# Optimization experiments

Hardware: AMD Instinct MI355X
Metric: run time of the kernel (lower is better)

The kernel has to match this reference:

```python
import jax, jax.numpy as jnp
import numpy as np

N_IN = 16384
G = 64            # input grid resolution
K_UP = 8          # 2^3 children per voxel for kernel=2 stride=2 generative transpose conv
N_OUT = N_IN * K_UP
G2 = 2 * G        # output grid resolution
NUMS = 32768      # top-k prune budget
C = 64


def _np_coords_and_maps():
    """Build voxel coords, the 27-offset kernel map on upsampled coords, and a fake GT mask."""
    rng = np.random.default_rng(0)
    flat = rng.choice(G ** 3, size=N_IN, replace=False)
    c = np.stack(np.unravel_index(flat, (G, G, G)), axis=1).astype(np.int64)  # [N_IN,3]
    offs2 = np.stack(np.meshgrid(*([[0, 1]] * 3), indexing='ij'), -1).reshape(-1, 3)  # [8,3]
    cu = (2 * c[:, None, :] + offs2[None]).reshape(-1, 3)  # [N_OUT,3], order n*8+k
    lut = np.full(G2 ** 3, N_OUT, dtype=np.int64)
    key = (cu[:, 0] * G2 + cu[:, 1]) * G2 + cu[:, 2]
    lut[key] = np.arange(N_OUT)
    offs3 = np.stack(np.meshgrid(*([[-1, 0, 1]] * 3), indexing='ij'), -1).reshape(-1, 3)  # [27,3]
    nbr = np.empty((27, N_OUT), np.int64)
    for k, d in enumerate(offs3):
        q = cu + d
        valid = ((q >= 0) & (q < G2)).all(1)
        qk = np.where(valid, (q[:, 0] * G2 + q[:, 1]) * G2 + q[:, 2], 0)
        nbr[k] = np.where(valid, lut[qk], N_OUT)  # N_OUT = sentinel 'missing'
    gt = rng.random(N_OUT) < 0.3  # isin(out.C, ground_truth.C) membership mask
    return nbr.astype(np.int32), gt


def setup_inputs() -> dict:
    key = jax.random.key(0)
    ks = jax.random.split(key, 10)
    nbr, gt = _np_coords_and_maps()
    s = 0.05
    rn = lambda k, shape: jax.random.normal(k, shape, jnp.float32) * s
    z = lambda shape: jnp.zeros(shape, jnp.float32)
    return {
        "x_feats": jax.random.normal(ks[0], (N_IN, C), jnp.float32),
        "Wup": rn(ks[1], (K_UP, C, C)), "bup": z((C,)),
        "Wc0": rn(ks[2], (27, C, C)), "bc0": z((C,)),
        "W00": rn(ks[3], (3, 27, C, C // 4)), "b00": z((3, C // 4)),
        "W01": rn(ks[4], (3, 27, C // 4, C // 2)), "b01": z((3, C // 2)),
        "W10": rn(ks[5], (3, C, C // 4)), "b10": z((3, C // 4)),
        "W11": rn(ks[6], (3, 27, C // 4, C // 4)), "b11": z((3, C // 4)),
        "W12": rn(ks[7], (3, C // 4, C // 2)), "b12": z((3, C // 2)),
        "Wcls": rn(ks[8], (27, C, 1)), "bcls": z((1,)),
        "nbr_idx": jnp.asarray(nbr), "mask_true": jnp.asarray(gt),
        "nums": NUMS,
    }


def sparse_conv(feats, nbr, W, b):
    """Gather-GEMM-scatter sparse conv: feats [N,Cin], nbr [K,N] (N = missing), W [K,Cin,Cout]."""
    fp = jnp.concatenate([feats, jnp.zeros((1, feats.shape[1]), feats.dtype)], axis=0)
    def body(acc, wn):
        Wk, nk = wn
        return acc + fp[nk] @ Wk, None
    acc0 = jnp.zeros((feats.shape[0], W.shape[-1]), feats.dtype)
    out, _ = jax.lax.scan(body, acc0, (W, nbr))
    return out + b


def reference(x_feats, Wup, bup, Wc0, bc0, W00, b00, W01, b01, W10, b10, W11, b11, W12, b12, Wcls, bcls, nbr_idx, mask_true, nums):
    # generative transpose conv k=2 s=2: each voxel emits 8 children (no overlaps)
    up = jnp.einsum('nc,kcd->nkd', x_feats, Wup).reshape(-1, Wup.shape[-1]) + bup  # [N_OUT,C]
    out = jax.nn.relu(up)
    out = jax.nn.relu(sparse_conv(out, nbr_idx, Wc0, bc0))
    for i in range(3):  # 3 InceptionResNet blocks
        o0 = sparse_conv(jax.nn.relu(sparse_conv(out, nbr_idx, W00[i], b00[i])), nbr_idx, W01[i], b01[i])
        t = jax.nn.relu(out @ W10[i] + b10[i])            # 1x1 conv
        t = jax.nn.relu(sparse_conv(t, nbr_idx, W11[i], b11[i]))
        o1 = t @ W12[i] + b12[i]                          # 1x1 conv
        out = jnp.concatenate([o0, o1], axis=1) + out
    out_cls = sparse_conv(out, nbr_idx, Wcls, bcls)       # [N_OUT,1]
    _, idx = jax.lax.top_k(out_cls[:, 0], nums)           # istopk
    mask = jnp.zeros((out.shape[0],), bool).at[idx].set(True) | mask_true  # topk + isin(GT)
    pruned = out * mask[:, None].astype(out.dtype)        # pruning as mask (static shape)
    return out_cls, pruned, mask
```

## Files before the change

kernel.cpp:

```cpp
#include <hip/hip_runtime.h>
#include <cstdint>

#define NOUTC 131072
#define NINC  16384

using uint = unsigned int;

__device__ __forceinline__ uint fkey(float v){
  uint u = __float_as_uint(v);
  return (u & 0x80000000u) ? ~u : (u | 0x80000000u);
}

template<int ROWS, int CIN, int COUT, int TR, int TC, int NK, bool IDENT, bool RELU, bool RESID>
__global__ __launch_bounds__(256)
void spconv(const float* __restrict__ feats,
            const int*   __restrict__ nbr,
            const float* __restrict__ Wg,
            const float* __restrict__ bias,
            const float* __restrict__ resid,
            float*       __restrict__ outp,
            int ostride, int coff)
{
  static_assert(TR == 4, "TR must be 4");
  static_assert((ROWS / TR) * (COUT / TC) == 256, "thread tiling must cover 256 threads");
  constexpr int TPR = 256 / ROWS;
  static_assert(ROWS * TPR == 256, "");
  constexpr int GV = CIN / (4 * TPR);
  static_assert(CIN % (4 * TPR) == 0, "");
  constexpr int STR = ROWS + 4;

  __shared__ float Wl[CIN * COUT];
  __shared__ float ft[CIN][STR];

  const int t    = threadIdx.x;
  const int base = blockIdx.x * ROWS;

  constexpr int CT = COUT / TC;
  const int tcc = (t % CT) * TC;
  const int trr = (t / CT) * TR;

  const int gr    = t / TPR;
  const int gpart = t % TPR;

  float acc[TR][TC];
  #pragma unroll
  for (int a = 0; a < TR; ++a)
    #pragma unroll
    for (int b = 0; b < TC; ++b) acc[a][b] = 0.f;

  for (int k = 0; k < NK; ++k) {
    #pragma unroll
    for (int i = t; i < CIN * COUT; i += 256) Wl[i] = Wg[k * CIN * COUT + i];
    int gidx = IDENT ? (base + gr) : nbr[(size_t)k * NOUTC + base + gr];
    const float4* src = reinterpret_cast<const float4*>(feats + (size_t)gidx * CIN) + gpart * GV;
    #pragma unroll
    for (int j = 0; j < GV; ++j) {
      float4 v = src[j];
      int ci = (gpart * GV + j) * 4;
      ft[ci + 0][gr] = v.x; ft[ci + 1][gr] = v.y;
      ft[ci + 2][gr] = v.z; ft[ci + 3][gr] = v.w;
    }
    __syncthreads();
    #pragma unroll
    for (int ci = 0; ci < CIN; ++ci) {
      float4 f = *reinterpret_cast<const float4*>(&ft[ci][trr]);
      float fv[4] = {f.x, f.y, f.z, f.w};
      float wv[TC];
      if constexpr (TC == 4) {
        float4 w = *reinterpret_cast<const float4*>(&Wl[ci * COUT + tcc]);
        wv[0] = w.x; wv[1] = w.y; wv[2] = w.z; wv[3] = w.w;
      } else {
        float2 w = *reinterpret_cast<const float2*>(&Wl[ci * COUT + tcc]);
        wv[0] = w.x; wv[1] = w.y;
      }
      #pragma unroll
      for (int a = 0; a < TR; ++a)
        #pragma unroll
        for (int b = 0; b < TC; ++b)
          acc[a][b] = fmaf(fv[a], wv[b], acc[a][b]);
    }
    __syncthreads();
  }

  #pragma unroll
  for (int a = 0; a < TR; ++a) {
    int rr = base + trr + a;
    float o[TC];
    #pragma unroll
    for (int b = 0; b < TC; ++b) {
      float v = acc[a][b] + bias[tcc + b];
      if (RELU) v = v > 0.f ? v : 0.f;
      o[b] = v;
    }
    if (RESID) {
      #pragma unroll
      for (int b = 0; b < TC; ++b)
        o[b] += resid[(size_t)rr * 64 + coff + tcc + b];
    }
    float* dst = outp + (size_t)rr * ostride + coff + tcc;
    if constexpr (TC == 4) {
      float4 w4 = {o[0], o[1], o[2], o[3]};
      *reinterpret_cast<float4*>(dst) = w4;
    } else {
      float2 w2 = {o[0], o[1]};
      *reinterpret_cast<float2*>(dst) = w2;
    }
  }
}

__global__ __launch_bounds__(256)
void upsample_kernel(const float* __restrict__ x, const float* __restrict__ Wup,
                     const float* __restrict__ bup, float* __restrict__ outp)
{
  __shared__ float Wl[64 * 64];
  __shared__ float xt[64][68];
  const int t    = threadIdx.x;
  const int tile = blockIdx.x >> 3;
  const int k    = blockIdx.x & 7;
  const int base = tile * 64;

  #pragma unroll
  for (int i = t; i < 4096; i += 256) Wl[i] = Wup[k * 4096 + i];
  {
    const int gr = t >> 2, gp = t & 3;
    const float4* src = reinterpret_cast<const float4*>(x + (size_t)(base + gr) * 64) + gp * 4;
    #pragma unroll
    for (int j = 0; j < 4; ++j) {
      float4 v = src[j];
      int ci = (gp * 4 + j) * 4;
      xt[ci + 0][gr] = v.x; xt[ci + 1][gr] = v.y;
      xt[ci + 2][gr] = v.z; xt[ci + 3][gr] = v.w;
    }
  }
  __syncthreads();
  const int tcc = (t % 16) * 4, trr = (t / 16) * 4;
  float acc[4][4];
  #pragma unroll
  for (int a = 0; a < 4; ++a)
    #pragma unroll
    for (int b = 0; b < 4; ++b) acc[a][b] = 0.f;
  #pragma unroll
  for (int ci = 0; ci < 64; ++ci) {
    float4 f = *reinterpret_cast<const float4*>(&xt[ci][trr]);
    float4 w = *reinterpret_cast<const float4*>(&Wl[ci * 64 + tcc]);
    float fv[4] = {f.x, f.y, f.z, f.w};
    float wv[4] = {w.x, w.y, w.z, w.w};
    #pragma unroll
    for (int a = 0; a < 4; ++a)
      #pragma unroll
      for (int b = 0; b < 4; ++b) acc[a][b] = fmaf(fv[a], wv[b], acc[a][b]);
  }
  #pragma unroll
  for (int a = 0; a < 4; ++a) {
    int n = base + trr + a;
    float4 o;
    float v0 = acc[a][0] + bup[tcc + 0]; o.x = v0 > 0.f ? v0 : 0.f;
    float v1 = acc[a][1] + bup[tcc + 1]; o.y = v1 > 0.f ? v1 : 0.f;
    float v2 = acc[a][2] + bup[tcc + 2]; o.z = v2 > 0.f ? v2 : 0.f;
    float v3 = acc[a][3] + bup[tcc + 3]; o.w = v3 > 0.f ? v3 : 0.f;
    *reinterpret_cast<float4*>(outp + ((size_t)n * 8 + k) * 64 + tcc) = o;
  }
}

__global__ __launch_bounds__(256)
void cls_kernel(const float* __restrict__ feats, const int* __restrict__ nbr,
                const float* __restrict__ Wcls, const float* __restrict__ bcls,
                float* __restrict__ out_cls)
{
  const int wave = threadIdx.x >> 6;
  const int lane = threadIdx.x & 63;
  float wreg[27];
  #pragma unroll
  for (int k = 0; k < 27; ++k) wreg[k] = Wcls[k * 64 + lane];
  const int base = blockIdx.x * 32 + wave * 8;
  for (int rr = 0; rr < 8; ++rr) {
    const int n = base + rr;
    float s = 0.f;
    #pragma unroll
    for (int k = 0; k < 27; ++k) {
      int idx = nbr[(size_t)k * NOUTC + n];
      s = fmaf(feats[(size_t)idx * 64 + lane], wreg[k], s);
    }
    #pragma unroll
    for (int off = 32; off >= 1; off >>= 1) s += __shfl_xor(s, off, 64);
    if (lane == 0) out_cls[n] = s + bcls[0];
  }
}

__global__ void init_kernel(uint* hist1, uint* hist2, int* tie_cnt, int* flag,
                            float* fa, float* fb, float* t0, float* t1)
{
  int i = blockIdx.x * 256 + threadIdx.x;
  if (i < 65536) hist1[i] = 0;
  else if (i < 131072) hist2[i - 65536] = 0;
  if (i == 0) { tie_cnt[0] = 0; flag[0] = 0; }
  if (i < 64) { fa[(size_t)NOUTC * 64 + i] = 0.f; fb[(size_t)NOUTC * 64 + i] = 0.f; }
  if (i < 16) { t0[(size_t)NOUTC * 16 + i] = 0.f; t1[(size_t)NOUTC * 16 + i] = 0.f; }
}

__global__ void detect_kernel(const unsigned char* __restrict__ mt, int* flag)
{
  int i = blockIdx.x * 256 + threadIdx.x;
  int p = i * 4 + 1;
  if (p < NOUTC && mt[p] != 0) flag[0] = 1;
}

__global__ void hist1_kernel(const float* __restrict__ cls, uint* __restrict__ hist)
{
  for (int i = blockIdx.x * blockDim.x + threadIdx.x; i < NOUTC; i += gridDim.x * blockDim.x)
    atomicAdd(&hist[fkey(cls[i]) >> 16], 1u);
}

__global__ void scan1_kernel(const uint* __restrict__ hist, const int* __restrict__ nums,
                             uint* __restrict__ res)
{
  __shared__ uint chunk[256];
  const int t = threadIdx.x;
  uint s = 0;
  for (int j = 0; j < 256; ++j) s += hist[t * 256 + j];
  chunk[t] = s;
  __syncthreads();
  if (t == 0) {
    uint k = (uint)nums[0];
    uint cum = 0; int c = 255;
    for (; c > 0; --c) { if (cum + chunk[c] >= k) break; cum += chunk[c]; }
    int B = c * 256; uint cum2 = cum;
    for (int b = c * 256 + 255; b >= c * 256; --b) {
      if (cum2 + hist[b] >= k) { B = b; break; }
      cum2 += hist[b];
    }
    res[0] = (uint)B; res[1] = cum2;
  }
}

__global__ void hist2_kernel(const float* __restrict__ cls, const uint* __restrict__ res1,
                             uint* __restrict__ hist)
{
  const uint B = res1[0];
  for (int i = blockIdx.x * blockDim.x + threadIdx.x; i < NOUTC; i += gridDim.x * blockDim.x) {
    uint key = fkey(cls[i]);
    if ((key >> 16) == B) atomicAdd(&hist[key & 0xffffu], 1u);
  }
}

__global__ void scan2_kernel(const uint* __restrict__ hist, const uint* __restrict__ res1,
                             const int* __restrict__ nums, uint* __restrict__ res2)
{
  __shared__ uint chunk[256];
  const int t = threadIdx.x;
  uint s = 0;
  for (int j = 0; j < 256; ++j) s += hist[t * 256 + j];
  chunk[t] = s;
  __syncthreads();
  if (t == 0) {
    uint k = (uint)nums[0];
    uint cum = res1[1]; int c = 255;
    for (; c > 0; --c) { if (cum + chunk[c] >= k) break; cum += chunk[c]; }
    int L = c * 256; uint cum2 = cum;
    for (int b = c * 256 + 255; b >= c * 256; --b) {
      if (cum2 + hist[b] >= k) { L = b; break; }
      cum2 += hist[b];
    }
    res2[0] = (res1[0] << 16) | (uint)L;
    res2[1] = k - cum2;
  }
}

__global__ void mark_kernel(const float* __restrict__ cls, const uint* __restrict__ res2,
                            unsigned char* __restrict__ msel, int* tie_cnt, int* tie_idx)
{
  const uint T = res2[0];
  for (int i = blockIdx.x * blockDim.x + threadIdx.x; i < NOUTC; i += gridDim.x * blockDim.x) {
    uint key = fkey(cls[i]);
    msel[i] = key > T ? 1 : 0;
    if (key == T) {
      int p = atomicAdd(tie_cnt, 1);
      if (p < 4096) tie_idx[p] = i;
    }
  }
}

__global__ void tie_kernel(const uint* __restrict__ res2, const int* __restrict__ tie_cnt,
                           const int* __restrict__ tie_idx, unsigned char* __restrict__ msel)
{
  int need = (int)res2[1];
  int cnt = tie_cnt[0]; if (cnt > 4096) cnt = 4096;
  if (need <= 0) return;
  if (cnt <= need) {
    for (int i = threadIdx.x; i < cnt; i += 256) msel[tie_idx[i]] = 1;
  } else {
    for (int i = threadIdx.x; i < cnt; i += 256) {
      int my = tie_idx[i];
      int rank = 0;
      for (int j = 0; j < cnt; ++j) rank += (tie_idx[j] < my) ? 1 : 0;
      if (rank < need) msel[my] = 1;
    }
  }
}

__global__ void prune_kernel(const float* __restrict__ feats, const unsigned char* __restrict__ msel,
                             const void* __restrict__ mtrue, const int* __restrict__ flag,
                             float* __restrict__ dout)
{
  const unsigned char* mb = (const unsigned char*)mtrue;
  const int* mi = (const int*)mtrue;
  const bool bytes = (flag[0] != 0);
  float* pruned = dout + NOUTC;
  float* maskf  = dout + NOUTC + (size_t)NOUTC * 64;
  const float4* src = reinterpret_cast<const float4*>(feats);
  float4* dst = reinterpret_cast<float4*>(pruned);
  const int total = NOUTC * 16;
  for (int i = blockIdx.x * blockDim.x + threadIdx.x; i < total; i += gridDim.x * blockDim.x) {
    int n = i >> 4;
    bool mt = bytes ? (mb[n] != 0) : (mi[n] != 0);
    bool m = (msel[n] != 0) || mt;
    float4 v = src[i];
    float4 z = {0.f, 0.f, 0.f, 0.f};
    dst[i] = m ? v : z;
    if ((i & 15) == 0) maskf[n] = m ? 1.f : 0.f;
  }
}

extern "C" void kernel_launch(void* const* d_in, const int* in_sizes, int n_in,
                              void* d_out, int out_size, void* d_ws, size_t ws_size,
                              hipStream_t stream)
{
  const float* x    = (const float*)d_in[0];
  const float* Wup  = (const float*)d_in[1];
  const float* bup  = (const float*)d_in[2];
  const float* Wc0  = (const float*)d_in[3];
  const float* bc0  = (const float*)d_in[4];
  const float* W00  = (const float*)d_in[5];
  const float* b00  = (const float*)d_in[6];
  const float* W01  = (const float*)d_in[7];
  const float* b01  = (const float*)d_in[8];
  const float* W10  = (const float*)d_in[9];
  const float* b10  = (const float*)d_in[10];
  const float* W11  = (const float*)d_in[11];
  const float* b11  = (const float*)d_in[12];
  const float* W12  = (const float*)d_in[13];
  const float* b12  = (const float*)d_in[14];
  const float* Wcls = (const float*)d_in[15];
  const float* bcls = (const float*)d_in[16];
  const int*   nbr  = (const int*)d_in[17];
  const void*  mtrue= d_in[18];
  const int*   nums = (const int*)d_in[19];

  float* dout = (float*)d_out;

  float* fa = (float*)d_ws;
  float* t0 = fa + (size_t)(NOUTC + 1) * 64;
  float* t1 = t0 + (size_t)(NOUTC + 1) * 16;
  uint*  hist1 = (uint*)(t1 + (size_t)(NOUTC + 1) * 16);
  uint*  hist2 = hist1 + 65536;
  uint*  res1  = hist2 + 65536;
  uint*  res2  = res1 + 2;
  int*   tie_cnt = (int*)(res2 + 2);
  int*   flag    = tie_cnt + 1;
  int*   tie_idx = flag + 1;
  unsigned char* msel = (unsigned char*)(tie_idx + 4096);
  float* fb = dout + NOUTC;

  init_kernel<<<512, 256, 0, stream>>>(hist1, hist2, tie_cnt, flag, fa, fb, t0, t1);
  detect_kernel<<<128, 256, 0, stream>>>((const unsigned char*)mtrue, flag);

  upsample_kernel<<<2048, 256, 0, stream>>>(x, Wup, bup, fa);
  spconv<64, 64, 64, 4, 4, 27, false, true, false>
      <<<NOUTC / 64, 256, 0, stream>>>(fa, nbr, Wc0, bc0, nullptr, fb, 64, 0);

  const float* cur = fb; float* nxt = fa;
  for (int i = 0; i < 3; ++i) {
    spconv<128, 64, 16, 4, 2, 27, false, true, false>
        <<<NOUTC / 128, 256, 0, stream>>>(cur, nbr, W00 + (size_t)i * 27 * 64 * 16,
                                          b00 + i * 16, nullptr, t0, 16, 0);
    spconv<128, 16, 32, 4, 4, 27, false, false, true>
        <<<NOUTC / 128, 256, 0, stream>>>(t0, nbr, W01 + (size_t)i * 27 * 16 * 32,
                                          b01 + i * 32, cur, nxt, 64, 0);
    spconv<128, 64, 16, 4, 2, 1, true, true, false>
        <<<NOUTC / 128, 256, 0, stream>>>(cur, nullptr, W10 + (size_t)i * 64 * 16,
                                          b10 + i * 16, nullptr, t1, 16, 0);
    spconv<128, 16, 16, 4, 2, 27, false, true, false>
        <<<NOUTC / 128, 256, 0, stream>>>(t1, nbr, W11 + (size_t)i * 27 * 16 * 16,
                                          b11 + i * 16, nullptr, t0, 16, 0);
    spconv<128, 16, 32, 4, 4, 1, true, false, true>
        <<<NOUTC / 128, 256, 0, stream>>>(t0, nullptr, W12 + (size_t)i * 16 * 32,
                                          b12 + i * 32, cur, nxt, 64, 32);
    float* tmp = (float*)cur; cur = nxt; nxt = tmp;
  }

  cls_kernel<<<NOUTC / 32, 256, 0, stream>>>(cur, nbr, Wcls, bcls, dout);

  hist1_kernel<<<512, 256, 0, stream>>>(dout, hist1);
  scan1_kernel<<<1, 256, 0, stream>>>(hist1, nums, res1);
  hist2_kernel<<<512, 256, 0, stream>>>(dout, res1, hist2);
  scan2_kernel<<<1, 256, 0, stream>>>(hist2, res1, nums, res2);
  mark_kernel<<<512, 256, 0, stream>>>(dout, res2, msel, tie_cnt, tie_idx);
  tie_kernel<<<1, 256, 0, stream>>>(res2, tie_cnt, tie_idx, msel);
  prune_kernel<<<4096, 256, 0, stream>>>(cur, msel, mtrue, flag, dout);
}
```

Measured before the change: 1.547 ms.

## Replace tiled spconv with one-row-per-thread fused kernels and split cls gather

Swaps the LDS-tiled sparse conv template for kernels where each thread owns one output row, keeps all output channels in registers and reads weights from global/uniform memory. Within each block it fuses the 3x3 and 1x1 branches: W00 and W10 share one gather pass, and W01, W11 and W12 plus the residual share another, which cuts launches and intermediate traffic. The classifier becomes a per-row dot product against all 27 weight slices followed by a scalar gather-sum. Block indices are swizzled. The cost is very high register pressure (64-float accumulators), lower occupancy, and weight loads no longer shared through LDS.

```diff
diff --git a/kernel.cpp b/kernel.cpp
--- a/kernel.cpp
+++ b/kernel.cpp
@@ -11,180 +11,274 @@
   return (u & 0x80000000u) ? ~u : (u | 0x80000000u);
 }
 
-template<int ROWS, int CIN, int COUT, int TR, int TC, int NK, bool IDENT, bool RELU, bool RESID>
-__global__ __launch_bounds__(256)
-void spconv(const float* __restrict__ feats,
-            const int*   __restrict__ nbr,
-            const float* __restrict__ Wg,
-            const float* __restrict__ bias,
-            const float* __restrict__ resid,
-            float*       __restrict__ outp,
-            int ostride, int coff)
-{
-  static_assert(TR == 4, "TR must be 4");
-  static_assert((ROWS / TR) * (COUT / TC) == 256, "thread tiling must cover 256 threads");
-  constexpr int TPR = 256 / ROWS;
-  static_assert(ROWS * TPR == 256, "");
-  constexpr int GV = CIN / (4 * TPR);
-  static_assert(CIN % (4 * TPR) == 0, "");
-  constexpr int STR = ROWS + 4;
-
-  __shared__ float Wl[CIN * COUT];
-  __shared__ float ft[CIN][STR];
-
-  const int t    = threadIdx.x;
-  const int base = blockIdx.x * ROWS;
-
-  constexpr int CT = COUT / TC;
-  const int tcc = (t % CT) * TC;
-  const int trr = (t / CT) * TR;
-
-  const int gr    = t / TPR;
-  const int gpart = t % TPR;
-
-  float acc[TR][TC];
-  #pragma unroll
-  for (int a = 0; a < TR; ++a)
+__device__ __forceinline__ int swz_row(int bx, int tid) {
+  return ((((bx & 7) << 6) | (bx >> 3)) << 8) + tid;
+}
+
+__global__ __launch_bounds__(256)
+void conv_c0_kernel(const float* __restrict__ feats, const int* __restrict__ nbr,
+                    const float* __restrict__ Wg, const float* __restrict__ bias,
+                    float* __restrict__ outp)
+{
+  const int n = swz_row(blockIdx.x, threadIdx.x);
+  float acc[64];
+  #pragma unroll
+  for (int i = 0; i < 64; ++i) acc[i] = 0.f;
+
+  for (int k = 0; k < 27; ++k) {
+    const int idx = nbr[(size_t)k * NOUTC + n];
+    const float4* src = reinterpret_cast<const float4*>(feats + (size_t)idx * 64);
+    const float* w = Wg + k * 4096;
+    #pragma unroll 1
+    for (int c = 0; c < 4; ++c) {
+      float4 a0 = src[c * 4 + 0], a1 = src[c * 4 + 1];
+      float4 a2 = src[c * 4 + 2], a3 = src[c * 4 + 3];
+      float fr[16];
+      fr[0]=a0.x; fr[1]=a0.y; fr[2]=a0.z; fr[3]=a0.w;
+      fr[4]=a1.x; fr[5]=a1.y; fr[6]=a1.z; fr[7]=a1.w;
+      fr[8]=a2.x; fr[9]=a2.y; fr[10]=a2.z; fr[11]=a2.w;
+      fr[12]=a3.x; fr[13]=a3.y; fr[14]=a3.z; fr[15]=a3.w;
+      const float* wc = w + c * 1024;
+      #pragma unroll
+      for (int u = 0; u < 16; ++u)
+        #pragma unroll
+        for (int co = 0; co < 64; ++co)
+          acc[co] = fmaf(fr[u], wc[u * 64 + co], acc[co]);
+    }
+  }
+
+  float* dst = outp + (size_t)n * 64;
+  #pragma unroll
+  for (int j = 0; j < 16; ++j) {
+    float4 o;
+    float v0 = acc[4*j+0] + bias[4*j+0]; o.x = v0 > 0.f ? v0 : 0.f;
+    float v1 = acc[4*j+1] + bias[4*j+1]; o.y = v1 > 0.f ? v1 : 0.f;
+    float v2 = acc[4*j+2] + bias[4*j+2]; o.z = v2 > 0.f ? v2 : 0.f;
+    float v3 = acc[4*j+3] + bias[4*j+3]; o.w = v3 > 0.f ? v3 : 0.f;
+    reinterpret_cast<float4*>(dst)[j] = o;
+  }
+}
+
+__global__ __launch_bounds__(256)
+void conv_A_kernel(const float* __restrict__ feats, const int* __restrict__ nbr,
+                   const float* __restrict__ W00i, const float* __restrict__ b00i,
+                   const float* __restrict__ W10i, const float* __restrict__ b10i,
+                   float* __restrict__ t0, float* __restrict__ t1)
+{
+  const int n = swz_row(blockIdx.x, threadIdx.x);
+  float acc0[16], acc1[16];
+  #pragma unroll
+  for (int i = 0; i < 16; ++i) { acc0[i] = 0.f; acc1[i] = 0.f; }
+
+  for (int k = 0; k < 27; ++k) {
+    const int idx = nbr[(size_t)k * NOUTC + n];
+    const float4* src = reinterpret_cast<const float4*>(feats + (size_t)idx * 64);
+    const float* w0 = W00i + k * 1024;
+    #pragma unroll 1
+    for (int c = 0; c < 4; ++c) {
+      float4 a0 = src[c * 4 + 0], a1 = src[c * 4 + 1];
+      float4 a2 = src[c * 4 + 2], a3 = src[c * 4 + 3];
+      float fr[16];
+      fr[0]=a0.x; fr[1]=a0.y; fr[2]=a0.z; fr[3]=a0.w;
+      fr[4]=a1.x; fr[5]=a1.y; fr[6]=a1.z; fr[7]=a1.w;
+      fr[8]=a2.x; fr[9]=a2.y; fr[10]=a2.z; fr[11]=a2.w;
+      fr[12]=a3.x; fr[13]=a3.y; fr[14]=a3.z; fr[15]=a3.w;
+      #pragma unroll
+      for (int u = 0; u < 16; ++u)
+        #pragma unroll
+        for (int co = 0; co < 16; ++co)
+          acc0[co] = fmaf(fr[u], w0[(c * 16 + u) * 16 + co], acc0[co]);
+      if (k == 13) {
+        #pragma unroll
+        for (int u = 0; u < 16; ++u)
+          #pragma unroll
+          for (int co = 0; co < 16; ++co)
+            acc1[co] = fmaf(fr[u], W10i[(c * 16 + u) * 16 + co], acc1[co]);
+      }
+    }
+  }
+
+  float* d0 = t0 + (size_t)n * 16;
+  float* d1 = t1 + (size_t)n * 16;
+  #pragma unroll
+  for (int j = 0; j < 4; ++j) {
+    float4 o0, o1;
+    float v;
+    v = acc0[4*j+0] + b00i[4*j+0]; o0.x = v > 0.f ? v : 0.f;
+    v = acc0[4*j+1] + b00i[4*j+1]; o0.y = v > 0.f ? v : 0.f;
+    v = acc0[4*j+2] + b00i[4*j+2]; o0.z = v > 0.f ? v : 0.f;
+    v = acc0[4*j+3] + b00i[4*j+3]; o0.w = v > 0.f ? v : 0.f;
+    v = acc1[4*j+0] + b10i[4*j+0]; o1.x = v > 0.f ? v : 0.f;
+    v = acc1[4*j+1] + b10i[4*j+1]; o1.y = v > 0.f ? v : 0.f;
+    v = acc1[4*j+2] + b10i[4*j+2]; o1.z = v > 0.f ? v : 0.f;
+    v = acc1[4*j+3] + b10i[4*j+3]; o1.w = v > 0.f ? v : 0.f;
+    reinterpret_cast<float4*>(d0)[j] = o0;
+    reinterpret_cast<float4*>(d1)[j] = o1;
+  }
+}
+
+__global__ __launch_bounds__(256)
+void conv_B_kernel(const float* __restrict__ t0, const float* __restrict__ t1,
+                   const float* __restrict__ cur, const int* __restrict__ nbr,
+                   const float* __restrict__ W01i, const float* __restrict__ b01i,
+                   const float* __restrict__ W11i, const float* __restrict__ b11i,
+                   const float* __restrict__ W12i, const float* __restrict__ b12i,
+                   float* __restrict__ nxt)
+{
+  const int n = swz_row(blockIdx.x, threadIdx.x);
+  float acc01[32], acc11[16];
+  #pragma unroll
+  for (int i = 0; i < 32; ++i) acc01[i] = 0.f;
+  #pragma unroll
+  for (int i = 0; i < 16; ++i) acc11[i] = 0.f;
+
+  for (int k = 0; k < 27; ++k) {
+    const int idx = nbr[(size_t)k * NOUTC + n];
+    const float4* s0 = reinterpret_cast<const float4*>(t0 + (size_t)idx * 16);
+    const float4* s1 = reinterpret_cast<const float4*>(t1 + (size_t)idx * 16);
+    float4 a0 = s0[0], a1 = s0[1], a2 = s0[2], a3 = s0[3];
+    float4 c0 = s1[0], c1 = s1[1], c2 = s1[2], c3 = s1[3];
+    float f0[16], f1[16];
+    f0[0]=a0.x; f0[1]=a0.y; f0[2]=a0.z; f0[3]=a0.w;
+    f0[4]=a1.x; f0[5]=a1.y; f0[6]=a1.z; f0[7]=a1.w;
+    f0[8]=a2.x; f0[9]=a2.y; f0[10]=a2.z; f0[11]=a2.w;
+    f0[12]=a3.x; f0[13]=a3.y; f0[14]=a3.z; f0[15]=a3.w;
+    f1[0]=c0.x; f1[1]=c0.y; f1[2]=c0.z; f1[3]=c0.w;
+    f1[4]=c1.x; f1[5]=c1.y; f1[6]=c1.z; f1[7]=c1.w;
+    f1[8]=c2.x; f1[9]=c2.y; f1[10]=c2.z; f1[11]=c2.w;
+    f1[12]=c3.x; f1[13]=c3.y; f1[14]=c3.z; f1[15]=c3.w;
+    const float* w01 = W01i + k * 512;
+    const float* w11 = W11i + k * 256;
     #pragma unroll
-    for (int b = 0; b < TC; ++b) acc[a][b] = 0.f;
-
-  for (int k = 0; k < NK; ++k) {
+    for (int u = 0; u < 16; ++u)
+      #pragma unroll
+      for (int co = 0; co < 32; ++co)
+        acc01[co] = fmaf(f0[u], w01[u * 32 + co], acc01[co]);
     #pragma unroll
-    for (int i = t; i < CIN * COUT; i += 256) Wl[i] = Wg[k * CIN * COUT + i];
-    int gidx = IDENT ? (base + gr) : nbr[(size_t)k * NOUTC + base + gr];
-    const float4* src = reinterpret_cast<const float4*>(feats + (size_t)gidx * CIN) + gpart * GV;
+    for (int u = 0; u < 16; ++u)
+      #pragma unroll
+      for (int co = 0; co < 16; ++co)
+        acc11[co] = fmaf(f1[u], w11[u * 16 + co], acc11[co]);
+  }
+
+  float t2[16];
+  #pragma unroll
+  for (int u = 0; u < 16; ++u) {
+    float v = acc11[u] + b11i[u];
+    t2[u] = v > 0.f ? v : 0.f;
+  }
+  float acc12[32];
+  #pragma unroll
+  for (int co = 0; co < 32; ++co) acc12[co] = b12i[co];
+  #pragma unroll
+  for (int u = 0; u < 16; ++u)
     #pragma unroll
-    for (int j = 0; j < GV; ++j) {
-      float4 v = src[j];
-      int ci = (gpart * GV + j) * 4;
-      ft[ci + 0][gr] = v.x; ft[ci + 1][gr] = v.y;
-      ft[ci + 2][gr] = v.z; ft[ci + 3][gr] = v.w;
-    }
-    __syncthreads();
+    for (int co = 0; co < 32; ++co)
+      acc12[co] = fmaf(t2[u], W12i[u * 32 + co], acc12[co]);
+
+  const float4* rs = reinterpret_cast<const float4*>(cur + (size_t)n * 64);
+  float* dst = nxt + (size_t)n * 64;
+  #pragma unroll
+  for (int j = 0; j < 8; ++j) {
+    float4 r = rs[j];
+    float4 o;
+    o.x = acc01[4*j+0] + b01i[4*j+0] + r.x;
+    o.y = acc01[4*j+1] + b01i[4*j+1] + r.y;
+    o.z = acc01[4*j+2] + b01i[4*j+2] + r.z;
+    o.w = acc01[4*j+3] + b01i[4*j+3] + r.w;
+    reinterpret_cast<float4*>(dst)[j] = o;
+  }
+  #pragma unroll
+  for (int j = 0; j < 8; ++j) {
+    float4 r = rs[8 + j];
+    float4 o;
+    o.x = acc12[4*j+0] + r.x;
+    o.y = acc12[4*j+1] + r.y;
+    o.z = acc12[4*j+2] + r.z;
+    o.w = acc12[4*j+3] + r.w;
+    reinterpret_cast<float4*>(dst)[8 + j] = o;
+  }
+}
+
+__global__ __launch_bounds__(256)
+void up2_kernel(const float* __restrict__ x, const float* __restrict__ Wup,
+                const float* __restrict__ bup, float* __restrict__ outp)
+{
+  const int k = blockIdx.x & 7;
+  const int n = (blockIdx.x >> 3) * 256 + threadIdx.x;
+  const float4* src = reinterpret_cast<const float4*>(x + (size_t)n * 64);
+  const float* w = Wup + k * 4096;
+  float acc[64];
+  #pragma unroll
+  for (int i = 0; i < 64; ++i) acc[i] = 0.f;
+  #pragma unroll 1
+  for (int c = 0; c < 4; ++c) {
+    float4 a0 = src[c * 4 + 0], a1 = src[c * 4 + 1];
+    float4 a2 = src[c * 4 + 2], a3 = src[c * 4 + 3];
+    float fr[16];
+    fr[0]=a0.x; fr[1]=a0.y; fr[2]=a0.z; fr[3]=a0.w;
+    fr[4]=a1.x; fr[5]=a1.y; fr[6]=a1.z; fr[7]=a1.w;
+    fr[8]=a2.x; fr[9]=a2.y; fr[10]=a2.z; fr[11]=a2.w;
+    fr[12]=a3.x; fr[13]=a3.y; fr[14]=a3.z; fr[15]=a3.w;
+    const float* wc = w + c * 1024;
     #pragma unroll
-    for (int ci = 0; ci < CIN; ++ci) {
-      float4 f = *reinterpret_cast<const float4*>(&ft[ci][trr]);
-      float fv[4] = {f.x, f.y, f.z, f.w};
-      float wv[TC];
-      if constexpr (TC == 4) {
-        float4 w = *reinterpret_cast<const float4*>(&Wl[ci * COUT + tcc]);
-        wv[0] = w.x; wv[1] = w.y; wv[2] = w.z; wv[3] = w.w;
-      } else {
-        float2 w = *reinterpret_cast<const float2*>(&Wl[ci * COUT + tcc]);
-        wv[0] = w.x; wv[1] = w.y;
-      }
+    for (int u = 0; u < 16; ++u)
       #pragma unroll
-      for (int a = 0; a < TR; ++a)
-        #pragma unroll
-        for (int b = 0; b < TC; ++b)
-          acc[a][b] = fmaf(fv[a], wv[b], acc[a][b]);
-    }
-    __syncthreads();
-  }
-
-  #pragma unroll
-  for (int a = 0; a < TR; ++a) {
-    int rr = base + trr + a;
-    float o[TC];
+      for (int co = 0; co < 64; ++co)
+        acc[co] = fmaf(fr[u], wc[u * 64 + co], acc[co]);
+  }
+  float* dst = outp + ((size_t)n * 8 + k) * 64;
+  #pragma unroll
+  for (int j = 0; j < 16; ++j) {
+    float4 o;
+    float v0 = acc[4*j+0] + bup[4*j+0]; o.x = v0 > 0.f ? v0 : 0.f;
+    float v1 = acc[4*j+1] + bup[4*j+1]; o.y = v1 > 0.f ? v1 : 0.f;
+    float v2 = acc[4*j+2] + bup[4*j+2]; o.z = v2 > 0.f ? v2 : 0.f;
+    float v3 = acc[4*j+3] + bup[4*j+3]; o.w = v3 > 0.f ? v3 : 0.f;
+    reinterpret_cast<float4*>(dst)[j] = o;
+  }
+}
+
+__global__ __launch_bounds__(256)
+void cls1_kernel(const float* __restrict__ feats, const float* __restrict__ Wcls,
+                 float* __restrict__ g)
+{
+  const int n = blockIdx.x * 256 + threadIdx.x;
+  if (blockIdx.x == 0 && threadIdx.x < 28) g[(size_t)NOUTC * 28 + threadIdx.x] = 0.f;
+  const float4* src = reinterpret_cast<const float4*>(feats + (size_t)n * 64);
+  float f[64];
+  #pragma unroll
+  for (int j = 0; j < 16; ++j) {
+    float4 a = src[j];
+    f[4*j+0]=a.x; f[4*j+1]=a.y; f[4*j+2]=a.z; f[4*j+3]=a.w;
+  }
+  #pragma unroll 1
+  for (int k = 0; k < 27; ++k) {
+    const float* w = Wcls + k * 64;
+    float s0 = 0.f, s1 = 0.f, s2 = 0.f, s3 = 0.f;
     #pragma unroll
-    for (int b = 0; b < TC; ++b) {
-      float v = acc[a][b] + bias[tcc + b];
-      if (RELU) v = v > 0.f ? v : 0.f;
-      o[b] = v;
-    }
-    if (RESID) {
-      #pragma unroll
-      for (int b = 0; b < TC; ++b)
-        o[b] += resid[(size_t)rr * 64 + coff + tcc + b];
-    }
-    float* dst = outp + (size_t)rr * ostride + coff + tcc;
-    if constexpr (TC == 4) {
-      float4 w4 = {o[0], o[1], o[2], o[3]};
-      *reinterpret_cast<float4*>(dst) = w4;
-    } else {
-      float2 w2 = {o[0], o[1]};
-      *reinterpret_cast<float2*>(dst) = w2;
-    }
-  }
-}
-
-__global__ __launch_bounds__(256)
-void upsample_kernel(const float* __restrict__ x, const float* __restrict__ Wup,
-                     const float* __restrict__ bup, float* __restrict__ outp)
-{
-  __shared__ float Wl[64 * 64];
-  __shared__ float xt[64][68];
-  const int t    = threadIdx.x;
-  const int tile = blockIdx.x >> 3;
-  const int k    = blockIdx.x & 7;
-  const int base = tile * 64;
-
-  #pragma unroll
-  for (int i = t; i < 4096; i += 256) Wl[i] = Wup[k * 4096 + i];
-  {
-    const int gr = t >> 2, gp = t & 3;
-    const float4* src = reinterpret_cast<const float4*>(x + (size_t)(base + gr) * 64) + gp * 4;
-    #pragma unroll
-    for (int j = 0; j < 4; ++j) {
-      float4 v = src[j];
-      int ci = (gp * 4 + j) * 4;
-      xt[ci + 0][gr] = v.x; xt[ci + 1][gr] = v.y;
-      xt[ci + 2][gr] = v.z; xt[ci + 3][gr] = v.w;
-    }
-  }
-  __syncthreads();
-  const int tcc = (t % 16) * 4, trr = (t / 16) * 4;
-  float acc[4][4];
-  #pragma unroll
-  for (int a = 0; a < 4; ++a)
-    #pragma unroll
-    for (int b = 0; b < 4; ++b) acc[a][b] = 0.f;
-  #pragma unroll
-  for (int ci = 0; ci < 64; ++ci) {
-    float4 f = *reinterpret_cast<const float4*>(&xt[ci][trr]);
-    float4 w = *reinterpret_cast<const float4*>(&Wl[ci * 64 + tcc]);
-    float fv[4] = {f.x, f.y, f.z, f.w};
-    float wv[4] = {w.x, w.y, w.z, w.w};
-    #pragma unroll
-    for (int a = 0; a < 4; ++a)
-      #pragma unroll
-      for (int b = 0; b < 4; ++b) acc[a][b] = fmaf(fv[a], wv[b], acc[a][b]);
-  }
-  #pragma unroll
-  for (int a = 0; a < 4; ++a) {
-    int n = base + trr + a;
-    float4 o;
-    float v0 = acc[a][0] + bup[tcc + 0]; o.x = v0 > 0.f ? v0 : 0.f;
-    float v1 = acc[a][1] + bup[tcc + 1]; o.y = v1 > 0.f ? v1 : 0.f;
-    float v2 = acc[a][2] + bup[tcc + 2]; o.z = v2 > 0.f ? v2 : 0.f;
-    float v3 = acc[a][3] + bup[tcc + 3]; o.w = v3 > 0.f ? v3 : 0.f;
-    *reinterpret_cast<float4*>(outp + ((size_t)n * 8 + k) * 64 + tcc) = o;
-  }
-}
-
-__global__ __launch_bounds__(256)
-void cls_kernel(const float* __restrict__ feats, const int* __restrict__ nbr,
-                const float* __restrict__ Wcls, const float* __restrict__ bcls,
-                float* __restrict__ out_cls)
-{
-  const int wave = threadIdx.x >> 6;
-  const int lane = threadIdx.x & 63;
-  float wreg[27];
-  #pragma unroll
-  for (int k = 0; k < 27; ++k) wreg[k] = Wcls[k * 64 + lane];
-  const int base = blockIdx.x * 32 + wave * 8;
-  for (int rr = 0; rr < 8; ++rr) {
-    const int n = base + rr;
-    float s = 0.f;
-    #pragma unroll
-    for (int k = 0; k < 27; ++k) {
-      int idx = nbr[(size_t)k * NOUTC + n];
-      s = fmaf(feats[(size_t)idx * 64 + lane], wreg[k], s);
-    }
-    #pragma unroll
-    for (int off = 32; off >= 1; off >>= 1) s += __shfl_xor(s, off, 64);
-    if (lane == 0) out_cls[n] = s + bcls[0];
-  }
+    for (int j = 0; j < 16; ++j) {
+      s0 = fmaf(f[j],      w[j],      s0);
+      s1 = fmaf(f[16 + j], w[16 + j], s1);
+      s2 = fmaf(f[32 + j], w[32 + j], s2);
+      s3 = fmaf(f[48 + j], w[48 + j], s3);
+    }
+    g[(size_t)n * 28 + k] = (s0 + s1) + (s2 + s3);
+  }
+}
+
+__global__ __launch_bounds__(256)
+void cls2_kernel(const float* __restrict__ g, const int* __restrict__ nbr,
+                 const float* __restrict__ bcls, float* __restrict__ out_cls)
+{
+  const int n = blockIdx.x * 256 + threadIdx.x;
+  float s = bcls[0];
+  #pragma unroll 1
+  for (int k = 0; k < 27; ++k) {
+    int idx = nbr[(size_t)k * NOUTC + n];
+    s += g[(size_t)idx * 28 + k];
+  }
+  out_cls[n] = s;
 }
 
 __global__ void init_kernel(uint* hist1, uint* hist2, int* tie_cnt, int* flag,
@@ -351,6 +445,7 @@
   float* fa = (float*)d_ws;
   float* t0 = fa + (size_t)(NOUTC + 1) * 64;
   float* t1 = t0 + (size_t)(NOUTC + 1) * 16;
+  float* g  = t0;
   uint*  hist1 = (uint*)(t1 + (size_t)(NOUTC + 1) * 16);
   uint*  hist2 = hist1 + 65536;
   uint*  res1  = hist2 + 65536;
@@ -364,31 +459,23 @@
   init_kernel<<<512, 256, 0, stream>>>(hist1, hist2, tie_cnt, flag, fa, fb, t0, t1);
   detect_kernel<<<128, 256, 0, stream>>>((const unsigned char*)mtrue, flag);
 
-  upsample_kernel<<<2048, 256, 0, stream>>>(x, Wup, bup, fa);
-  spconv<64, 64, 64, 4, 4, 27, false, true, false>
-      <<<NOUTC / 64, 256, 0, stream>>>(fa, nbr, Wc0, bc0, nullptr, fb, 64, 0);
+  up2_kernel<<<512, 256, 0, stream>>>(x, Wup, bup, fa);
+  conv_c0_kernel<<<512, 256, 0, stream>>>(fa, nbr, Wc0, bc0, fb);
 
   const float* cur = fb; float* nxt = fa;
   for (int i = 0; i < 3; ++i) {
-    spconv<128, 64, 16, 4, 2, 27, false, true, false>
-        <<<NOUTC / 128, 256, 0, stream>>>(cur, nbr, W00 + (size_t)i * 27 * 64 * 16,
-                                          b00 + i * 16, nullptr, t0, 16, 0);
-    spconv<128, 16, 32, 4, 4, 27, false, false, true>
-        <<<NOUTC / 128, 256, 0, stream>>>(t0, nbr, W01 + (size_t)i * 27 * 16 * 32,
-                                          b01 + i * 32, cur, nxt, 64, 0);
-    spconv<128, 64, 16, 4, 2, 1, true, true, false>
-        <<<NOUTC / 128, 256, 0, stream>>>(cur, nullptr, W10 + (size_t)i * 64 * 16,
-                                          b10 + i * 16, nullptr, t1, 16, 0);
-    spconv<128, 16, 16, 4, 2, 27, false, true, false>
-        <<<NOUTC / 128, 256, 0, stream>>>(t1, nbr, W11 + (size_t)i * 27 * 16 * 16,
-                                          b11 + i * 16, nullptr, t0, 16, 0);
-    spconv<128, 16, 32, 4, 4, 1, true, false, true>
-        <<<NOUTC / 128, 256, 0, stream>>>(t0, nullptr, W12 + (size_t)i * 16 * 32,
-                                          b12 + i * 32, cur, nxt, 64, 32);
+    conv_A_kernel<<<512, 256, 0, stream>>>(cur, nbr,
+        W00 + (size_t)i * 27 * 1024, b00 + i * 16,
+        W10 + (size_t)i * 1024,      b10 + i * 16, t0, t1);
+    conv_B_kernel<<<512, 256, 0, stream>>>(t0, t1, cur, nbr,
+        W01 + (size_t)i * 27 * 512, b01 + i * 32,
+        W11 + (size_t)i * 27 * 256, b11 + i * 16,
+        W12 + (size_t)i * 512,      b12 + i * 32, nxt);
     float* tmp = (float*)cur; cur = nxt; nxt = tmp;
   }
 
-  cls_kernel<<<NOUTC / 32, 256, 0, stream>>>(cur, nbr, Wcls, bcls, dout);
+  cls1_kernel<<<512, 256, 0, stream>>>(cur, Wcls, g);
+  cls2_kernel<<<512, 256, 0, stream>>>(g, nbr, bcls, dout);
 
   hist1_kernel<<<512, 256, 0, stream>>>(dout, hist1);
   scan1_kernel<<<1, 256, 0, stream>>>(hist1, nums, res1);
```

Result: slower. 2.647 ms (+71.1%).
